# Kernel optimization log

Measured on AMD Instinct MI355X. Metric: run time of the kernel, lower is better.

Reference implementation:

```python
import jax, jax.numpy as jnp
import numpy as np

BATCH = 8192
IN_FEATURES = 128
OUT_FEATURES = 256
GRID_SIZE = 20
ORDER = 3
L = GRID_SIZE + ORDER  # coeffs length per edge = 23


def setup_inputs() -> dict:
    key = jax.random.key(0)
    kx, kc = jax.random.split(key)
    x = jax.random.normal(kx, (BATCH, IN_FEATURES), dtype=jnp.float32)
    # fused per-edge B-spline coefficients: [out_features, in_features, grid_size+order]
    coeffs = jax.random.normal(kc, (OUT_FEATURES, IN_FEATURES, L), dtype=jnp.float32) * 0.1
    return {"x": x, "coeffs": coeffs}


def reference(x, coeffs):
    # x: [B, I], coeffs: [O, I, L]
    O, I, Lc = coeffs.shape
    B = x.shape[0]
    s = jax.nn.sigmoid(x)                      # x_clamped in (0, 1)
    idx = s * (GRID_SIZE - 1)                  # fractional bin index in [0, 19)
    k = idx.astype(jnp.int32)                  # trunc == floor since idx >= 0
    w1 = idx - k.astype(x.dtype)
    w0 = 1.0 - w1
    k0 = jnp.clip(k, 0, Lc - 1)                # [B, I]
    k1 = jnp.clip(k + 1, 0, Lc - 1)
    # Build sparse interpolation weights [B, I, L] (two nonzeros per (b, j)),
    # then contract against the shared coefficient tensor in one fused reduce:
    # out[b, i] = sum_j c[i, j, k0[b,j]] * w0[b,j] + c[i, j, k1[b,j]] * w1[b,j]
    brow = jnp.arange(B)[:, None]
    jcol = jnp.arange(I)[None, :]
    W = jnp.zeros((B, I, Lc), dtype=x.dtype)
    W = W.at[brow, jcol, k0].add(w0)
    W = W.at[brow, jcol, k1].add(w1)
    return jnp.einsum('bjl,ijl->bi', W, coeffs)  # [B, O]
```

## Files before the change

### kernel.cpp

```cpp
#include <hip/hip_runtime.h>
#include <hip/hip_fp16.h>

#define BATCH 8192
#define IN_F 128
#define OUT_F 256
#define LC 23
#define BROW 768
#define JPW 16

typedef _Float16 f16x8 __attribute__((ext_vector_type(8)));
typedef float f32x4 __attribute__((ext_vector_type(4)));
typedef _Float16 half2v __attribute__((ext_vector_type(2)));

__global__ __launch_bounds__(256) void prep_fast(
    const float* __restrict__ coeffs, char* __restrict__ cp2) {
    __shared__ float slab[256 * LC];
    const size_t base = (size_t)blockIdx.x * 256;
    {
        const float4* g4 = reinterpret_cast<const float4*>(coeffs + base * LC);
        float4* s4 = reinterpret_cast<float4*>(slab);
        for (int it = threadIdx.x; it < (256 * LC) / 4; it += 256)
            s4[it] = g4[it];
    }
    __syncthreads();
    const int t = (int)base + threadIdx.x;
    const int i = t >> 7;
    const int j = t & 127;
    const float* my = slab + threadIdx.x * LC;
    const int g = i >> 4;
    const int col = i & 15;
    char* row = cp2 + (size_t)(j * 16 + g) * BROW + col * 16;
    f16x8 w0, w1, w2;
#pragma unroll
    for (int e = 0; e < 8; ++e) {
        w0[e] = (_Float16)my[e];
        w1[e] = (_Float16)my[8 + e];
        w2[e] = (e < 4) ? (_Float16)my[16 + e] : (_Float16)0.0f;
    }
    *reinterpret_cast<f16x8*>(row) = w0;
    *reinterpret_cast<f16x8*>(row + 256) = w1;
    *reinterpret_cast<f16x8*>(row + 512) = w2;
}

__global__ __launch_bounds__(512, 4) void kan_mfma8(
    const float* __restrict__ x, const char* __restrict__ cp2,
    float* __restrict__ out) {
    __shared__ uint2 mlds[IN_F][64];

    const int tid = threadIdx.x;
    const int lane = tid & 63;
    const int ks = tid >> 6;
    const int l15 = lane & 15;
    const int q = lane >> 4;
    const int q4 = q * 4;
    const int qc = (q < 3) ? q : 2;

    int wg = (blockIdx.x & 7) * 64 + (blockIdx.x >> 3);
    const int mb = wg >> 2;
    const int bn = wg & 3;
    const int b0 = mb * 64;

    {
        const int row = lane;
        const int jb = ks * 16;
        const float4* xr = reinterpret_cast<const float4*>(
            x + (size_t)(b0 + row) * IN_F + jb);
#pragma unroll
        for (int u = 0; u < 4; ++u) {
            float4 xv = xr[u];
#pragma unroll
            for (int e = 0; e < 4; ++e) {
                float xvv = (e == 0) ? xv.x : (e == 1) ? xv.y
                           : (e == 2) ? xv.z : xv.w;
                float s = 1.0f / (1.0f + __expf(-xvv));
                float idxf = s * 19.0f;
                int k = (int)idxf;
                k = (k > 18) ? 18 : k;
                float w1 = idxf - (float)k;
                float w0 = 1.0f - w1;
                unsigned u0 = __half_as_ushort(__float2half(w0));
                unsigned u1 = __half_as_ushort(__float2half(w1));
                unsigned lo, hi;
                if (k & 1) { lo = u0 << 16; hi = u1; }
                else       { lo = u0 | (u1 << 16); hi = 0u; }
                unsigned P = (unsigned)(k >> 1);
                mlds[jb + u * 4 + e][row] = uint2{lo, hi | (P << 16)};
            }
        }
    }
    __syncthreads();

    const int j0 = ks * JPW;
    const char* bbase = cp2 + (size_t)(bn * 4) * BROW + qc * 256 + l15 * 16;
    auto bld = [&](int j, int nf) {
        return *reinterpret_cast<const f16x8*>(
            bbase + (size_t)(j * 16 + nf) * BROW);
    };

    f32x4 acc[4][4];
#pragma unroll
    for (int mf = 0; mf < 4; ++mf)
#pragma unroll
        for (int nf = 0; nf < 4; ++nf) acc[mf][nf] = f32x4{0.f, 0.f, 0.f, 0.f};

    f16x8 rc[4], rn[4];
#pragma unroll
    for (int h = 0; h < 4; ++h) rc[h] = bld(j0, h);

    auto step = [&](f16x8 (&cur)[4], f16x8 (&nxt)[4], int j, int jn) {
#pragma unroll
        for (int h = 0; h < 4; ++h) nxt[h] = bld(jn, h);
#pragma unroll
        for (int mf = 0; mf < 4; ++mf) {
            uint2 m = mlds[j][mf * 16 + l15];
            unsigned lo = m.x;
            unsigned hi = m.y & 0xFFFFu;
            int d = (int)(m.y >> 16) - q4;
            union { uint32_t u[4]; f16x8 h; } au;
#pragma unroll
            for (int r = 0; r < 4; ++r) {
                uint32_t v = (d == r) ? lo : 0u;
                v = (d == r - 1) ? hi : v;
                au.u[r] = v;
            }
#pragma unroll
            for (int nf = 0; nf < 4; ++nf)
                acc[mf][nf] = __builtin_amdgcn_mfma_f32_16x16x32_f16(
                    au.h, cur[nf], acc[mf][nf], 0, 0, 0);
        }
    };

    for (int jj = 0; jj < JPW; jj += 2) {
        step(rc, rn, j0 + jj, j0 + jj + 1);
        step(rn, rc, j0 + jj + 1, j0 + ((jj + 2) & (JPW - 1)));
    }

    __syncthreads();
    float* red = reinterpret_cast<float*>(&mlds[0][0]);
#pragma unroll
    for (int p = 0; p < 2; ++p) {
        if (p) __syncthreads();
#pragma unroll
        for (int mf = 0; mf < 4; ++mf)
#pragma unroll
            for (int t = 0; t < 2; ++t)
#pragma unroll
                for (int r = 0; r < 4; ++r) {
                    int colsw = (t * 16 + l15 + (q & 1) * 16) & 31;
                    red[ks * 2048 + (mf * 16 + q4 + r) * 32 + colsw] =
                        acc[mf][p * 2 + t][r];
                }
        __syncthreads();
#pragma unroll
        for (int it = 0; it < 4; ++it) {
            int idx = it * 512 + tid;
            int row = idx >> 5;
            int col = idx & 31;
            int colsw = (col + ((row >> 2) & 1) * 16) & 31;
            float s = 0.f;
#pragma unroll
            for (int w = 0; w < 8; ++w) s += red[w * 2048 + row * 32 + colsw];
            out[(size_t)(b0 + row) * OUT_F + bn * 64 + p * 32 + col] = s;
        }
    }
}

__device__ __forceinline__ float dot2_acc(unsigned cbits, unsigned wbits,
                                          float acc) {
#if __has_builtin(__builtin_amdgcn_fdot2)
    union { unsigned u; half2v h; } c, w;
    c.u = cbits; w.u = wbits;
    return __builtin_amdgcn_fdot2(c.h, w.h, acc, false);
#else
    __half2 hc = *reinterpret_cast<const __half2*>(&cbits);
    __half2 hw = *reinterpret_cast<const __half2*>(&wbits);
    float2 fc = __half22float2(hc);
    float2 fw = __half22float2(hw);
    return acc + fc.x * fw.x + fc.y * fw.y;
#endif
}

__global__ __launch_bounds__(256) void build_ctg_kernel(
    const float* __restrict__ coeffs, unsigned short* __restrict__ ctg) {
    int tid = blockIdx.x * 256 + threadIdx.x;
    int qq = tid & 63;
    int k = (tid >> 6) % LC;
    int j = tid / (64 * LC);
    if (j >= IN_F) return;
    int k1 = (k + 1 < LC) ? (k + 1) : (LC - 1);
    union { unsigned short h[8]; uint4 v; } u;
#pragma unroll
    for (int c = 0; c < 4; ++c) {
        int i = qq * 4 + c;
        const float* base = coeffs + ((size_t)i * IN_F + j) * LC;
        u.h[2 * c]     = __half_as_ushort(__float2half(base[k]));
        u.h[2 * c + 1] = __half_as_ushort(__float2half(base[k1]));
    }
    reinterpret_cast<uint4*>(ctg)[tid] = u.v;
}

__global__ __launch_bounds__(256) void kan_main_kernel(
    const float* __restrict__ x, const char* __restrict__ ctg,
    float* __restrict__ out) {
    __shared__ unsigned metas[4][2 * IN_F];
    const int wave = threadIdx.x >> 6;
    const int lane = threadIdx.x & 63;
    const int b = blockIdx.x * 4 + wave;
    float2 xv = reinterpret_cast<const float2*>(x + (size_t)b * IN_F)[lane];
    uint4 m;
#pragma unroll
    for (int t = 0; t < 2; ++t) {
        float xs = t ? xv.y : xv.x;
        float s = 1.0f / (1.0f + __expf(-xs));
        float idxf = s * 19.0f;
        int k = (int)idxf;
        k = (k > 18) ? 18 : k;
        float w1 = idxf - (float)k;
        float w0 = 1.0f - w1;
        int j = 2 * lane + t;
        unsigned off = (unsigned)((j * LC + k) << 10);
        half2v w; w[0] = (_Float16)w0; w[1] = (_Float16)w1;
        unsigned wbits = *reinterpret_cast<unsigned*>(&w);
        if (t == 0) { m.x = off; m.y = wbits; }
        else        { m.z = off; m.w = wbits; }
    }
    reinterpret_cast<uint4*>(&metas[wave][0])[lane] = m;
    __syncthreads();
    const unsigned lanebase = lane * 16;
    const uint4* mrow = reinterpret_cast<const uint4*>(&metas[wave][0]);
    float acc0 = 0.f, acc1 = 0.f, acc2 = 0.f, acc3 = 0.f;
#pragma unroll 8
    for (int j2 = 0; j2 < IN_F / 2; ++j2) {
        uint4 mm = mrow[j2];
        {
            const uint4 e = *reinterpret_cast<const uint4*>(
                ctg + (size_t)(lanebase + mm.x));
            acc0 = dot2_acc(e.x, mm.y, acc0);
            acc1 = dot2_acc(e.y, mm.y, acc1);
            acc2 = dot2_acc(e.z, mm.y, acc2);
            acc3 = dot2_acc(e.w, mm.y, acc3);
        }
        {
            const uint4 e = *reinterpret_cast<const uint4*>(
                ctg + (size_t)(lanebase + mm.z));
            acc0 = dot2_acc(e.x, mm.w, acc0);
            acc1 = dot2_acc(e.y, mm.w, acc1);
            acc2 = dot2_acc(e.z, mm.w, acc2);
            acc3 = dot2_acc(e.w, mm.w, acc3);
        }
    }
    float4 r = make_float4(acc0, acc1, acc2, acc3);
    reinterpret_cast<float4*>(out + (size_t)b * OUT_F)[lane] = r;
}

extern "C" void kernel_launch(void* const* d_in, const int* in_sizes, int n_in,
                              void* d_out, int out_size, void* d_ws,
                              size_t ws_size, hipStream_t stream) {
    const float* x = (const float*)d_in[0];
    const float* coeffs = (const float*)d_in[1];
    float* out = (float*)d_out;

    const size_t cp2_bytes = (size_t)IN_F * 16 * BROW;
    const size_t ctg_bytes = (size_t)IN_F * LC * 64 * 16;

    if (d_ws != nullptr && ws_size >= cp2_bytes) {
        char* cp2 = (char*)d_ws;
        prep_fast<<<128, 256, 0, stream>>>(coeffs, cp2);
        kan_mfma8<<<512, 512, 0, stream>>>(x, cp2, out);
    } else if (d_ws != nullptr && ws_size >= ctg_bytes) {
        char* ctg = (char*)d_ws;
        const int totalA = IN_F * LC * 64;
        build_ctg_kernel<<<(totalA + 255) / 256, 256, 0, stream>>>(
            coeffs, (unsigned short*)ctg);
        kan_main_kernel<<<BATCH / 4, 256, 0, stream>>>(x, ctg, out);
    } else {
        kan_main_kernel<<<BATCH / 4, 256, 0, stream>>>(x, (const char*)d_ws,
                                                       out);
    }
}
```

Baseline: 30.13 us.

## Retile KAN MFMA kernel to 16 batch rows per block with LDS A-table

The main kernel is restructured so each block handles 16 batch rows across all 256 outputs, with 4 waves splitting the output columns and 2 waves splitting the input features. The A operand is no longer built per lane from packed metadata and selects. It is written into a zeroed LDS table once per 32-feature chunk and read back with one vector load per MFMA. This removes the per-fragment select logic and shrinks the cross-wave reduction to two partials. The cost is that each coefficient fragment is now reused over only 16 batch rows instead of 64, which raises global/L2 traffic for B, and there are extra zeroing passes and barriers per chunk.

```diff
diff --git a/kernel.cpp b/kernel.cpp
--- a/kernel.cpp
+++ b/kernel.cpp
@@ -6,7 +6,6 @@
 #define OUT_F 256
 #define LC 23
 #define BROW 768
-#define JPW 16
 
 typedef _Float16 f16x8 __attribute__((ext_vector_type(8)));
 typedef float f32x4 __attribute__((ext_vector_type(4)));
@@ -42,126 +41,100 @@
     *reinterpret_cast<f16x8*>(row + 512) = w2;
 }
 
-__global__ __launch_bounds__(512, 4) void kan_mfma8(
+__global__ __launch_bounds__(512, 4) void kan_mfma12(
     const float* __restrict__ x, const char* __restrict__ cp2,
     float* __restrict__ out) {
-    __shared__ uint2 mlds[IN_F][64];
+    __shared__ unsigned atab[32][16][16];
 
     const int tid = threadIdx.x;
     const int lane = tid & 63;
-    const int ks = tid >> 6;
+    const int wv = tid >> 6;
+    const int bn = wv & 3;
+    const int ks = wv >> 2;
     const int l15 = lane & 15;
     const int q = lane >> 4;
     const int q4 = q * 4;
     const int qc = (q < 3) ? q : 2;
 
-    int wg = (blockIdx.x & 7) * 64 + (blockIdx.x >> 3);
-    const int mb = wg >> 2;
-    const int bn = wg & 3;
-    const int b0 = mb * 64;
-
-    {
-        const int row = lane;
-        const int jb = ks * 16;
-        const float4* xr = reinterpret_cast<const float4*>(
-            x + (size_t)(b0 + row) * IN_F + jb);
-#pragma unroll
-        for (int u = 0; u < 4; ++u) {
-            float4 xv = xr[u];
-#pragma unroll
-            for (int e = 0; e < 4; ++e) {
-                float xvv = (e == 0) ? xv.x : (e == 1) ? xv.y
-                           : (e == 2) ? xv.z : xv.w;
-                float s = 1.0f / (1.0f + __expf(-xvv));
-                float idxf = s * 19.0f;
-                int k = (int)idxf;
-                k = (k > 18) ? 18 : k;
-                float w1 = idxf - (float)k;
-                float w0 = 1.0f - w1;
-                unsigned u0 = __half_as_ushort(__float2half(w0));
-                unsigned u1 = __half_as_ushort(__float2half(w1));
-                unsigned lo, hi;
-                if (k & 1) { lo = u0 << 16; hi = u1; }
-                else       { lo = u0 | (u1 << 16); hi = 0u; }
-                unsigned P = (unsigned)(k >> 1);
-                mlds[jb + u * 4 + e][row] = uint2{lo, hi | (P << 16)};
-            }
-        }
-    }
+    const int b0 = blockIdx.x * 16;
+
+    const int s_row = tid >> 5;
+    const int s_jj = tid & 31;
+
+    f32x4 acc[4];
+#pragma unroll
+    for (int nf = 0; nf < 4; ++nf) acc[nf] = f32x4{0.f, 0.f, 0.f, 0.f};
+
+    const char* bbase = cp2 + (size_t)(bn * 4) * BROW + qc * 256 + l15 * 16;
+
+    for (int c = 0; c < 4; ++c) {
+        uint4* az = reinterpret_cast<uint4*>(&atab[0][0][0]);
+#pragma unroll
+        for (int w = 0; w < 4; ++w)
+            az[tid + w * 512] = uint4{0u, 0u, 0u, 0u};
+        __syncthreads();
+        {
+            const int j = c * 32 + s_jj;
+            float xv = x[(size_t)(b0 + s_row) * IN_F + j];
+            float s = 1.0f / (1.0f + __expf(-xv));
+            float idxf = s * 19.0f;
+            int k = (int)idxf;
+            k = (k > 18) ? 18 : k;
+            float w1 = idxf - (float)k;
+            float w0 = 1.0f - w1;
+            unsigned u0 = __half_as_ushort(__float2half(w0));
+            unsigned u1 = __half_as_ushort(__float2half(w1));
+            unsigned lo, hi;
+            if (k & 1) { lo = u0 << 16; hi = u1; }
+            else       { lo = u0 | (u1 << 16); hi = 0u; }
+            int P = k >> 1;
+            atab[s_jj][s_row][P] = lo;
+            atab[s_jj][s_row][P + 1] = hi;
+        }
+        __syncthreads();
+        const int jbase = ks * 16;
+        auto bldc = [&](int jj2, int nf) {
+            return *reinterpret_cast<const f16x8*>(
+                bbase + (size_t)((c * 32 + jj2) * 16 + nf) * BROW);
+        };
+        f16x8 rc[4], rn[4];
+#pragma unroll
+        for (int h = 0; h < 4; ++h) rc[h] = bldc(jbase, h);
+#pragma unroll 2
+        for (int jj2 = 0; jj2 < 16; ++jj2) {
+            const int jnx = jbase + ((jj2 + 1) & 15);
+#pragma unroll
+            for (int h = 0; h < 4; ++h) rn[h] = bldc(jnx, h);
+            union { uint4 v; f16x8 h; } au;
+            au.v = *reinterpret_cast<const uint4*>(
+                &atab[jbase + jj2][l15][q4]);
+#pragma unroll
+            for (int nf = 0; nf < 4; ++nf)
+                acc[nf] = __builtin_amdgcn_mfma_f32_16x16x32_f16(
+                    au.h, rc[nf], acc[nf], 0, 0, 0);
+#pragma unroll
+            for (int h = 0; h < 4; ++h) rc[h] = rn[h];
+        }
+        __syncthreads();
+    }
+
+    float* red = reinterpret_cast<float*>(&atab[0][0][0]);
+#pragma unroll
+    for (int nf = 0; nf < 4; ++nf)
+#pragma unroll
+        for (int r = 0; r < 4; ++r)
+            red[wv * 1024 + (q4 + r) * 64 + nf * 16 + l15] = acc[nf][r];
     __syncthreads();
-
-    const int j0 = ks * JPW;
-    const char* bbase = cp2 + (size_t)(bn * 4) * BROW + qc * 256 + l15 * 16;
-    auto bld = [&](int j, int nf) {
-        return *reinterpret_cast<const f16x8*>(
-            bbase + (size_t)(j * 16 + nf) * BROW);
-    };
-
-    f32x4 acc[4][4];
-#pragma unroll
-    for (int mf = 0; mf < 4; ++mf)
-#pragma unroll
-        for (int nf = 0; nf < 4; ++nf) acc[mf][nf] = f32x4{0.f, 0.f, 0.f, 0.f};
-
-    f16x8 rc[4], rn[4];
-#pragma unroll
-    for (int h = 0; h < 4; ++h) rc[h] = bld(j0, h);
-
-    auto step = [&](f16x8 (&cur)[4], f16x8 (&nxt)[4], int j, int jn) {
-#pragma unroll
-        for (int h = 0; h < 4; ++h) nxt[h] = bld(jn, h);
-#pragma unroll
-        for (int mf = 0; mf < 4; ++mf) {
-            uint2 m = mlds[j][mf * 16 + l15];
-            unsigned lo = m.x;
-            unsigned hi = m.y & 0xFFFFu;
-            int d = (int)(m.y >> 16) - q4;
-            union { uint32_t u[4]; f16x8 h; } au;
-#pragma unroll
-            for (int r = 0; r < 4; ++r) {
-                uint32_t v = (d == r) ? lo : 0u;
-                v = (d == r - 1) ? hi : v;
-                au.u[r] = v;
-            }
-#pragma unroll
-            for (int nf = 0; nf < 4; ++nf)
-                acc[mf][nf] = __builtin_amdgcn_mfma_f32_16x16x32_f16(
-                    au.h, cur[nf], acc[mf][nf], 0, 0, 0);
-        }
-    };
-
-    for (int jj = 0; jj < JPW; jj += 2) {
-        step(rc, rn, j0 + jj, j0 + jj + 1);
-        step(rn, rc, j0 + jj + 1, j0 + ((jj + 2) & (JPW - 1)));
-    }
-
-    __syncthreads();
-    float* red = reinterpret_cast<float*>(&mlds[0][0]);
-#pragma unroll
-    for (int p = 0; p < 2; ++p) {
-        if (p) __syncthreads();
-#pragma unroll
-        for (int mf = 0; mf < 4; ++mf)
-#pragma unroll
-            for (int t = 0; t < 2; ++t)
-#pragma unroll
-                for (int r = 0; r < 4; ++r) {
-                    int colsw = (t * 16 + l15 + (q & 1) * 16) & 31;
-                    red[ks * 2048 + (mf * 16 + q4 + r) * 32 + colsw] =
-                        acc[mf][p * 2 + t][r];
-                }
-        __syncthreads();
-#pragma unroll
-        for (int it = 0; it < 4; ++it) {
-            int idx = it * 512 + tid;
-            int row = idx >> 5;
-            int col = idx & 31;
-            int colsw = (col + ((row >> 2) & 1) * 16) & 31;
-            float s = 0.f;
-#pragma unroll
-            for (int w = 0; w < 8; ++w) s += red[w * 2048 + row * 32 + colsw];
-            out[(size_t)(b0 + row) * OUT_F + bn * 64 + p * 32 + col] = s;
-        }
+#pragma unroll
+    for (int it = 0; it < 8; ++it) {
+        int idx = it * 512 + tid;
+        int row = idx >> 8;
+        int col = idx & 255;
+        int cb = col >> 6;
+        int cc = col & 63;
+        float s = red[cb * 1024 + row * 64 + cc] +
+                  red[(4 + cb) * 1024 + row * 64 + cc];
+        out[(size_t)(b0 + row) * OUT_F + col] = s;
     }
 }
 
@@ -266,7 +239,7 @@
     if (d_ws != nullptr && ws_size >= cp2_bytes) {
         char* cp2 = (char*)d_ws;
         prep_fast<<<128, 256, 0, stream>>>(coeffs, cp2);
-        kan_mfma8<<<512, 512, 0, stream>>>(x, cp2, out);
+        kan_mfma12<<<512, 512, 0, stream>>>(x, cp2, out);
     } else if (d_ws != nullptr && ws_size >= ctg_bytes) {
         char* ctg = (char*)d_ws;
         const int totalA = IN_F * LC * 64;
```

Result: slower. 45.72 us (+51.8%).
